# Kernel optimization log

Hardware: AMD Instinct MI355X
Metric: run time of the kernel (lower is better)

Reference implementation:

```python
import jax, jax.numpy as jnp
import numpy as np

HEAD_DIM = 32
KERNEL = 3
DILATION = 2


def _unfold(x, k, dil):
    """torch.nn.Unfold with stride=1, padding=dil*(k-1)//2.
    x: [B, C, H, W] -> patches [B, C, k*k, H, W] (kernel positions row-major,
    channel-major overall, matching torch's (B, C*k*k, L) layout)."""
    B, C, H, W = x.shape
    pad = dil * (k - 1) // 2
    xp = jnp.pad(x, ((0, 0), (0, 0), (pad, pad), (pad, pad)))
    patches = jnp.stack(
        [xp[:, :, i * dil:i * dil + H, j * dil:j * dil + W]
         for i in range(k) for j in range(k)],
        axis=2,
    )
    return patches  # [B, C, k*k, H, W]


def setup_inputs() -> dict:
    key = jax.random.key(0)
    kq, kk, kv = jax.random.split(key, 3)
    shape = (8, 384, 56, 56)
    return {
        "q": jax.random.normal(kq, shape, dtype=jnp.float32),
        "k": jax.random.normal(kk, shape, dtype=jnp.float32),
        "v": jax.random.normal(kv, shape, dtype=jnp.float32),
    }


def reference(q, k, v):
    B, d, H, W = q.shape
    h = d // HEAD_DIM
    N = H * W
    k2 = KERNEL * KERNEL
    scale = HEAD_DIM ** (-0.5)

    # q: [B, h, N, hd]
    qr = q.reshape(B, h, HEAD_DIM, N).transpose(0, 1, 3, 2)
    # k patches: [B, h, hd, k2, N]
    kp = _unfold(k, KERNEL, DILATION).reshape(B, h, HEAD_DIM, k2, N)
    attn = jnp.einsum('bhnd,bhdkn->bhnk', qr, kp) * scale
    attn = jax.nn.softmax(attn, axis=-1)
    # v patches: [B, h, hd, k2, N]
    vp = _unfold(v, KERNEL, DILATION).reshape(B, h, HEAD_DIM, k2, N)
    out = jnp.einsum('bhnk,bhdkn->bhnd', attn, vp)  # [B, h, N, hd]
    # transpose(1,2) then reshape(B, H, W, d)
    return out.transpose(0, 2, 1, 3).reshape(B, H, W, d)
```

## Files before the change

kernel.cpp:

```cpp
#include <hip/hip_runtime.h>

#define HD 32
#define HALF 16
#define NHEADS 12
#define HH 56
#define WW 56
#define NN (HH * WW)
#define BB 8
#define CC (HD * NHEADS)
#define TILE_N 128
#define SCALE 0.17677669529663689f

__global__ __launch_bounds__(256) void dilate_attn_kernel(
    const float* __restrict__ q,
    const float* __restrict__ k,
    const float* __restrict__ v,
    float* __restrict__ out)
{
    const int xi = threadIdx.x;
    const int half = threadIdx.y;
    const int n = blockIdx.x * TILE_N + xi;
    const int bh = blockIdx.y;
    const int b = bh / NHEADS;
    const int head = bh - b * NHEADS;
    const bool active = (n < NN);

    const int y = n / WW;
    const int x = n - y * WW;

    const size_t base = ((size_t)b * CC + (size_t)head * HD + (size_t)half * HALF) * NN;

    __shared__ float part[2][TILE_N][9];

    float qv[HALF];
    if (active) {
        const float* qb = q + base + n;
#pragma unroll
        for (int d = 0; d < HALF; ++d) qv[d] = qb[(size_t)d * NN];
    }

    float lg[9];
#pragma unroll
    for (int t = 0; t < 9; ++t) {
        const int dy = ((t / 3) - 1) * 2;
        const int dx = ((t % 3) - 1) * 2;
        const int ny = y + dy;
        const int nx = x + dx;
        float s = 0.f;
        if (active && (unsigned)ny < HH && (unsigned)nx < WW) {
            const float* kb = k + base + (size_t)(ny * WW + nx);
#pragma unroll
            for (int d = 0; d < HALF; ++d) s = fmaf(qv[d], kb[(size_t)d * NN], s);
        }
        lg[t] = s;
        part[half][xi][t] = s;
    }
    __syncthreads();

    {
        const int other = 1 - half;
#pragma unroll
        for (int t = 0; t < 9; ++t)
            lg[t] = (lg[t] + part[other][xi][t]) * SCALE;
    }
    float m = lg[0];
#pragma unroll
    for (int t = 1; t < 9; ++t) m = fmaxf(m, lg[t]);
    float wsum = 0.f;
#pragma unroll
    for (int t = 0; t < 9; ++t) { lg[t] = __expf(lg[t] - m); wsum += lg[t]; }
    const float inv = 1.f / wsum;

    float acc[HALF];
#pragma unroll
    for (int d = 0; d < HALF; ++d) acc[d] = 0.f;
#pragma unroll
    for (int t = 0; t < 9; ++t) {
        const int dy = ((t / 3) - 1) * 2;
        const int dx = ((t % 3) - 1) * 2;
        const int ny = y + dy;
        const int nx = x + dx;
        if (active && (unsigned)ny < HH && (unsigned)nx < WW) {
            const float w = lg[t] * inv;
            const float* vb = v + base + (size_t)(ny * WW + nx);
#pragma unroll
            for (int d = 0; d < HALF; ++d) acc[d] = fmaf(w, vb[(size_t)d * NN], acc[d]);
        }
    }

    if (active) {
        float* ob = out + (((size_t)b * HH + y) * WW + x) * CC
                    + (size_t)head * HD + (size_t)half * HALF;
#pragma unroll
        for (int d = 0; d < HALF; d += 4) {
            float4 val = make_float4(acc[d], acc[d + 1], acc[d + 2], acc[d + 3]);
            *reinterpret_cast<float4*>(ob + d) = val;
        }
    }
}

extern "C" void kernel_launch(void* const* d_in, const int* in_sizes, int n_in,
                              void* d_out, int out_size, void* d_ws, size_t ws_size,
                              hipStream_t stream) {
    const float* q = (const float*)d_in[0];
    const float* k = (const float*)d_in[1];
    const float* v = (const float*)d_in[2];
    float* out = (float*)d_out;

    dim3 block(TILE_N, 2);
    dim3 grid((NN + TILE_N - 1) / TILE_N, BB * NHEADS);
    dilate_attn_kernel<<<grid, block, 0, stream>>>(q, k, v, out);
}
```

Baseline: 185.2 us.

## Process pixel pairs per thread with float2 loads and split channels into quarters

Each thread now handles two horizontally adjacent pixels and loads q, k, v as float2, so global load instructions are wider. The head dimension is split across four thread rows of 8 channels instead of two of 16, and partial logits are reduced through a larger shared buffer. The aim is fewer memory transactions per useful byte and more threads working on the channel dimension. Because W is even, x0 and the dilation offsets stay even, so a neighbour pair is either entirely inside or entirely outside the image and the float2 boundary test is exact. The cost is a heavier shared-memory reduction across four partials and more logit work duplicated per channel quarter.

```diff
diff --git a/kernel.cpp b/kernel.cpp
--- a/kernel.cpp
+++ b/kernel.cpp
@@ -1,14 +1,16 @@
 #include <hip/hip_runtime.h>
 
 #define HD 32
-#define HALF 16
+#define QCH 8
+#define NQ 4
 #define NHEADS 12
 #define HH 56
 #define WW 56
 #define NN (HH * WW)
 #define BB 8
 #define CC (HD * NHEADS)
-#define TILE_N 128
+#define PAIRS_PER_BLK 64
+#define NPAIRS (NN / 2)
 #define SCALE 0.17677669529663689f
 
 __global__ __launch_bounds__(256) void dilate_attn_kernel(
@@ -18,84 +20,110 @@
     float* __restrict__ out)
 {
     const int xi = threadIdx.x;
-    const int half = threadIdx.y;
-    const int n = blockIdx.x * TILE_N + xi;
+    const int qtr = threadIdx.y;
+    const int pair = blockIdx.x * PAIRS_PER_BLK + xi;
+    const bool active = (pair < NPAIRS);
+    const int n0 = 2 * pair;
+    const int y = n0 / WW;
+    const int x0 = n0 - y * WW;
+
     const int bh = blockIdx.y;
     const int b = bh / NHEADS;
     const int head = bh - b * NHEADS;
-    const bool active = (n < NN);
 
-    const int y = n / WW;
-    const int x = n - y * WW;
+    const size_t base = ((size_t)b * CC + (size_t)head * HD + (size_t)qtr * QCH) * NN;
 
-    const size_t base = ((size_t)b * CC + (size_t)head * HD + (size_t)half * HALF) * NN;
+    __shared__ float2 part[NQ][9][PAIRS_PER_BLK];
 
-    __shared__ float part[2][TILE_N][9];
-
-    float qv[HALF];
+    float2 qv[QCH];
+#pragma unroll
+    for (int d = 0; d < QCH; ++d) qv[d] = make_float2(0.f, 0.f);
     if (active) {
-        const float* qb = q + base + n;
+        const float* qb = q + base + n0;
 #pragma unroll
-        for (int d = 0; d < HALF; ++d) qv[d] = qb[(size_t)d * NN];
+        for (int d = 0; d < QCH; ++d)
+            qv[d] = *reinterpret_cast<const float2*>(qb + (size_t)d * NN);
     }
 
-    float lg[9];
+    float2 lg[9];
 #pragma unroll
     for (int t = 0; t < 9; ++t) {
         const int dy = ((t / 3) - 1) * 2;
         const int dx = ((t % 3) - 1) * 2;
         const int ny = y + dy;
-        const int nx = x + dx;
-        float s = 0.f;
-        if (active && (unsigned)ny < HH && (unsigned)nx < WW) {
+        const int nx = x0 + dx;
+        float2 s = make_float2(0.f, 0.f);
+        if (active && (unsigned)ny < HH && (unsigned)nx < (WW - 1)) {
             const float* kb = k + base + (size_t)(ny * WW + nx);
 #pragma unroll
-            for (int d = 0; d < HALF; ++d) s = fmaf(qv[d], kb[(size_t)d * NN], s);
+            for (int d = 0; d < QCH; ++d) {
+                const float2 kv = *reinterpret_cast<const float2*>(kb + (size_t)d * NN);
+                s.x = fmaf(qv[d].x, kv.x, s.x);
+                s.y = fmaf(qv[d].y, kv.y, s.y);
+            }
         }
         lg[t] = s;
-        part[half][xi][t] = s;
+        part[qtr][t][xi] = s;
     }
     __syncthreads();
 
-    {
-        const int other = 1 - half;
 #pragma unroll
-        for (int t = 0; t < 9; ++t)
-            lg[t] = (lg[t] + part[other][xi][t]) * SCALE;
+    for (int o = 1; o < NQ; ++o) {
+        const int oq = (qtr + o) & 3;
+#pragma unroll
+        for (int t = 0; t < 9; ++t) {
+            const float2 p = part[oq][t][xi];
+            lg[t].x += p.x;
+            lg[t].y += p.y;
+        }
     }
-    float m = lg[0];
 #pragma unroll
-    for (int t = 1; t < 9; ++t) m = fmaxf(m, lg[t]);
-    float wsum = 0.f;
+    for (int t = 0; t < 9; ++t) { lg[t].x *= SCALE; lg[t].y *= SCALE; }
+
+    float mx = lg[0].x, my = lg[0].y;
 #pragma unroll
-    for (int t = 0; t < 9; ++t) { lg[t] = __expf(lg[t] - m); wsum += lg[t]; }
-    const float inv = 1.f / wsum;
+    for (int t = 1; t < 9; ++t) { mx = fmaxf(mx, lg[t].x); my = fmaxf(my, lg[t].y); }
+    float sx = 0.f, sy = 0.f;
+#pragma unroll
+    for (int t = 0; t < 9; ++t) {
+        lg[t].x = __expf(lg[t].x - mx); sx += lg[t].x;
+        lg[t].y = __expf(lg[t].y - my); sy += lg[t].y;
+    }
+    const float ix = 1.f / sx, iy = 1.f / sy;
 
-    float acc[HALF];
+    float2 acc[QCH];
 #pragma unroll
-    for (int d = 0; d < HALF; ++d) acc[d] = 0.f;
+    for (int d = 0; d < QCH; ++d) acc[d] = make_float2(0.f, 0.f);
 #pragma unroll
     for (int t = 0; t < 9; ++t) {
         const int dy = ((t / 3) - 1) * 2;
         const int dx = ((t % 3) - 1) * 2;
         const int ny = y + dy;
-        const int nx = x + dx;
-        if (active && (unsigned)ny < HH && (unsigned)nx < WW) {
-            const float w = lg[t] * inv;
+        const int nx = x0 + dx;
+        if (active && (unsigned)ny < HH && (unsigned)nx < (WW - 1)) {
+            const float wx = lg[t].x * ix;
+            const float wy = lg[t].y * iy;
             const float* vb = v + base + (size_t)(ny * WW + nx);
 #pragma unroll
-            for (int d = 0; d < HALF; ++d) acc[d] = fmaf(w, vb[(size_t)d * NN], acc[d]);
+            for (int d = 0; d < QCH; ++d) {
+                const float2 vv = *reinterpret_cast<const float2*>(vb + (size_t)d * NN);
+                acc[d].x = fmaf(wx, vv.x, acc[d].x);
+                acc[d].y = fmaf(wy, vv.y, acc[d].y);
+            }
         }
     }
 
     if (active) {
-        float* ob = out + (((size_t)b * HH + y) * WW + x) * CC
-                    + (size_t)head * HD + (size_t)half * HALF;
-#pragma unroll
-        for (int d = 0; d < HALF; d += 4) {
-            float4 val = make_float4(acc[d], acc[d + 1], acc[d + 2], acc[d + 3]);
-            *reinterpret_cast<float4*>(ob + d) = val;
-        }
+        float* ob0 = out + ((size_t)b * NN + n0) * CC + (size_t)head * HD + (size_t)qtr * QCH;
+        float* ob1 = ob0 + CC;
+        float4 s0 = make_float4(acc[0].x, acc[1].x, acc[2].x, acc[3].x);
+        float4 s1 = make_float4(acc[4].x, acc[5].x, acc[6].x, acc[7].x);
+        float4 s2 = make_float4(acc[0].y, acc[1].y, acc[2].y, acc[3].y);
+        float4 s3 = make_float4(acc[4].y, acc[5].y, acc[6].y, acc[7].y);
+        reinterpret_cast<float4*>(ob0)[0] = s0;
+        reinterpret_cast<float4*>(ob0)[1] = s1;
+        reinterpret_cast<float4*>(ob1)[0] = s2;
+        reinterpret_cast<float4*>(ob1)[1] = s3;
     }
 }
 
@@ -107,7 +135,7 @@
     const float* v = (const float*)d_in[2];
     float* out = (float*)d_out;
 
-    dim3 block(TILE_N, 2);
-    dim3 grid((NN + TILE_N - 1) / TILE_N, BB * NHEADS);
+    dim3 block(PAIRS_PER_BLK, NQ);
+    dim3 grid((NPAIRS + PAIRS_PER_BLK - 1) / PAIRS_PER_BLK, BB * NHEADS);
     dilate_attn_kernel<<<grid, block, 0, stream>>>(q, k, v, out);
 }
```

Result: no change. 185.9 us (+0.4%).
